# Kernel tuning notes

Measured on AMD Instinct MI355X. Metric: run time of the kernel, lower is better.

The kernel has to match this reference:

```python
import jax, jax.numpy as jnp
import numpy as np

B, Hs, Ws, ENC = 128, 14, 14, 2048
ATT, EMB, DEC, V, L = 512, 512, 512, 30000, 22


def setup_inputs() -> dict:
    key = jax.random.key(0)
    ks = jax.random.split(key, 16)
    u = lambda k, shape, a: jax.random.uniform(k, shape, jnp.float32, -a, a)
    cap_len_rest = jax.random.randint(ks[2], (B - 1, 1), 2, L + 1)
    caption_lengths = jnp.concatenate([jnp.array([[L]], dtype=cap_len_rest.dtype), cap_len_rest], axis=0)
    return {
        "encoder_out": jax.random.normal(ks[0], (B, Hs, Ws, ENC), jnp.float32),
        "encoded_captions": jax.random.randint(ks[1], (B, L), 0, V),
        "caption_lengths": caption_lengths,
        # learned parameters
        "emb_table": u(ks[3], (V, EMB), 0.1),
        "We": u(ks[4], (ENC, ATT), 0.02), "be": jnp.zeros((ATT,), jnp.float32),
        "Wd": u(ks[5], (DEC, ATT), 0.02), "bd": jnp.zeros((ATT,), jnp.float32),
        "wf": u(ks[6], (ATT,), 0.02), "bf": jnp.zeros((), jnp.float32),
        "W_ih": u(ks[7], (4 * DEC, EMB + ENC), 0.02), "b_ih": jnp.zeros((4 * DEC,), jnp.float32),
        "W_hh": u(ks[8], (4 * DEC, DEC), 0.02), "b_hh": jnp.zeros((4 * DEC,), jnp.float32),
        "W_fc": u(ks[9], (DEC, V), 0.1), "b_fc": jnp.zeros((V,), jnp.float32),
    }


def reference(encoder_out, encoded_captions, caption_lengths,
              emb_table, We, be, Wd, bd, wf, bf,
              W_ih, b_ih, W_hh, b_hh, W_fc, b_fc):
    Bsz = encoder_out.shape[0]
    enc = encoder_out.reshape(Bsz, -1, encoder_out.shape[-1])  # [B, P, ENC]
    lens = caption_lengths[:, 0]
    sort_ind = jnp.argsort(-lens)  # descending, stable
    lens = lens[sort_ind]
    enc = enc[sort_ind]
    caps = encoded_captions[sort_ind]
    emb = emb_table[caps]  # [B, L, EMB]
    dec_lens = lens - 1
    T = caps.shape[1] - 1  # static max(decode_lengths) (max length present in batch)
    D = W_hh.shape[1]

    attn1 = enc @ We + be  # [B, P, ATT], loop-invariant
    h0 = jnp.zeros((Bsz, D), enc.dtype)
    c0 = jnp.zeros((Bsz, D), enc.dtype)

    def step(carry, xs):
        h, c = carry
        emb_t, active = xs  # [B, EMB], [B] bool
        attn2 = h @ Wd + bd  # [B, ATT]
        e = jnp.einsum('bpa,a->bp', jax.nn.relu(attn1 + attn2[:, None, :]), wf) + bf
        alpha = jax.nn.softmax(e, axis=1)  # [B, P]
        ctx = jnp.einsum('bp,bpe->be', alpha, enc)  # [B, ENC]
        x = jnp.concatenate([emb_t, ctx], axis=1)
        gates = x @ W_ih.T + b_ih + h @ W_hh.T + b_hh
        i, f, g, o = jnp.split(gates, 4, axis=1)  # PyTorch LSTM gate order
        c_new = jax.nn.sigmoid(f) * c + jax.nn.sigmoid(i) * jnp.tanh(g)
        h_new = jax.nn.sigmoid(o) * jnp.tanh(c_new)
        m = active[:, None]
        h = jnp.where(m, h_new, h)
        c = jnp.where(m, c_new, c)
        out_t = jnp.where(m, h_new @ W_fc + b_fc, 0.0)  # [B, V]
        alpha_t = jnp.where(m, alpha, 0.0)
        return (h, c), (out_t, alpha_t)

    ts = jnp.arange(T)
    active = ts[:, None] < dec_lens[None, :]  # [T, B]
    emb_steps = jnp.transpose(emb[:, :T], (1, 0, 2))  # [T, B, EMB]
    (_, _), (outs, alphas) = jax.lax.scan(step, (h0, c0), (emb_steps, active))
    outputs = jnp.transpose(outs, (1, 0, 2))  # [B, T, V]
    alphas = jnp.transpose(alphas, (1, 0, 2))  # [B, T, P]
    return outputs, caps, dec_lens, alphas, sort_ind
```

## Files before the change

### kernel.cpp

```cpp
#include <hip/hip_runtime.h>
#include <cstdint>
#include <cstddef>

#define B_    128
#define P_    196
#define ENC_  2048
#define ATT_  512
#define DEC_  512
#define EMB_  512
#define V_    30000
#define L_    22
#define T_    21
#define KGATE (EMB_ + ENC_ + DEC_)
#define NGATE (4*DEC_)
#define KS    8
#define LDSK  40

typedef unsigned short u16;
typedef unsigned int   u32;
typedef float f32x4 __attribute__((ext_vector_type(4)));
typedef short s16x8 __attribute__((ext_vector_type(8)));

__device__ __forceinline__ u16 f2bf(float f){
  u32 u = __float_as_uint(f);
  u = (u + 0x7fffu + ((u >> 16) & 1u)) >> 16;
  return (u16)u;
}
__device__ __forceinline__ float bf2f(u16 h){
  return __uint_as_float(((u32)h) << 16);
}

template<int MODE>
__global__ __launch_bounds__(256)
void gemm_bf16(const u16* __restrict__ A, int lda,
               const u16* __restrict__ Bm, int N, int K, int M,
               const float* __restrict__ bias,
               u16* __restrict__ outb,
               float* __restrict__ outp,
               const int* __restrict__ declens)
{
  __shared__ __align__(16) u16 As[64*LDSK];
  __shared__ __align__(16) u16 Bs[64*LDSK];
  __shared__ __align__(16) float Cs[64*68];

  const int tid = threadIdx.x;
  const int nt = blockIdx.x * 64;
  const int mt = blockIdx.y * 64;
  int k0 = 0, k1 = K;
  if (MODE == 1){ int kl = K / KS; k0 = blockIdx.z * kl; k1 = k0 + kl; }

  f32x4 acc[4];
  #pragma unroll
  for (int s = 0; s < 4; s++) acc[s] = f32x4{0.f,0.f,0.f,0.f};

  const int am = tid >> 2;
  const int ak = (tid & 3) * 8;
  const int bk = tid >> 3;
  const int bn = (tid & 7) * 8;
  const int wv = tid >> 6;
  const int ln = tid & 63;
  const int qd = ln >> 4;
  const int lm = ln & 15;

  for (int kc = k0; kc < k1; kc += 32){
    uint4 av = *reinterpret_cast<const uint4*>(A + (size_t)(mt + am) * lda + kc + ak);
    *reinterpret_cast<uint4*>(&As[am * LDSK + ak]) = av;
    u16 bv[8];
    bool inb = true;
    if (MODE == 2) inb = (nt + bn + 8 <= N);
    if (inb){
      uint4 bq = *reinterpret_cast<const uint4*>(Bm + (size_t)(kc + bk) * N + nt + bn);
      bv[0]=(u16)(bq.x&0xffff); bv[1]=(u16)(bq.x>>16);
      bv[2]=(u16)(bq.y&0xffff); bv[3]=(u16)(bq.y>>16);
      bv[4]=(u16)(bq.z&0xffff); bv[5]=(u16)(bq.z>>16);
      bv[6]=(u16)(bq.w&0xffff); bv[7]=(u16)(bq.w>>16);
    } else {
      #pragma unroll
      for (int j=0;j<8;j++) bv[j]=0;
    }
    #pragma unroll
    for (int j=0;j<8;j++) Bs[(bn + j) * LDSK + bk] = bv[j];
    __syncthreads();

    s16x8 af = *reinterpret_cast<const s16x8*>(&As[(wv*16 + lm) * LDSK + qd*8]);
    #pragma unroll
    for (int s=0;s<4;s++){
      s16x8 bfr = *reinterpret_cast<const s16x8*>(&Bs[(s*16 + lm) * LDSK + qd*8]);
      acc[s] = __builtin_amdgcn_mfma_f32_16x16x32_bf16(af, bfr, acc[s], 0, 0, 0);
    }
    __syncthreads();
  }

  #pragma unroll
  for (int s=0;s<4;s++)
    #pragma unroll
    for (int r=0;r<4;r++)
      Cs[(wv*16 + qd*4 + r)*68 + s*16 + lm] = acc[s][r];
  __syncthreads();

  const int row = tid >> 2;
  const int cs0 = (tid & 3) * 16;
  if (MODE == 0){
    __align__(16) u16 pack[16];
    #pragma unroll
    for (int j=0;j<16;j++)
      pack[j] = f2bf(Cs[row*68 + cs0 + j] + bias[nt + cs0 + j]);
    uint4* dst = reinterpret_cast<uint4*>(outb + (size_t)(mt+row)*N + nt + cs0);
    dst[0] = *reinterpret_cast<uint4*>(pack);
    dst[1] = *reinterpret_cast<uint4*>(pack + 8);
  } else if (MODE == 1){
    float* dst = outp + (size_t)blockIdx.z * M * N + (size_t)(mt+row)*N + nt + cs0;
    #pragma unroll
    for (int j=0;j<4;j++){
      float4 v = { Cs[row*68+cs0+4*j], Cs[row*68+cs0+4*j+1],
                   Cs[row*68+cs0+4*j+2], Cs[row*68+cs0+4*j+3] };
      reinterpret_cast<float4*>(dst)[j] = v;
    }
  } else {
    int r = mt + row;
    int ti = r >> 7;
    int bb = r & 127;
    bool act = ti < declens[bb];
    float* dst = outp + ((size_t)bb * T_ + ti) * (size_t)V_ + nt + cs0;
    #pragma unroll
    for (int j=0;j<16;j++){
      int col = nt + cs0 + j;
      if (col < N) dst[j] = act ? (Cs[row*68 + cs0 + j] + bias[col]) : 0.f;
    }
  }
}

__global__ void cvt_bf16(const float* __restrict__ in, u16* __restrict__ out, int n4){
  int i = blockIdx.x * blockDim.x + threadIdx.x;
  int stride = gridDim.x * blockDim.x;
  for (; i < n4; i += stride){
    float4 v = reinterpret_cast<const float4*>(in)[i];
    __align__(8) u16 p[4] = {f2bf(v.x), f2bf(v.y), f2bf(v.z), f2bf(v.w)};
    reinterpret_cast<uint2*>(out)[i] = *reinterpret_cast<uint2*>(p);
  }
}

__global__ void build_bigb(const float* __restrict__ Wih, const float* __restrict__ Whh,
                           u16* __restrict__ out)
{
  __shared__ float tile[32][33];
  int k0 = blockIdx.x * 32, n0 = blockIdx.y * 32;
  int tx = threadIdx.x, ty = threadIdx.y;
  #pragma unroll
  for (int j=0;j<4;j++){
    int nl = ty + j*8;
    int n = n0 + nl, k = k0 + tx;
    float v = (k0 < 2560) ? Wih[(size_t)n*2560 + k] : Whh[(size_t)n*512 + (k - 2560)];
    tile[nl][tx] = v;
  }
  __syncthreads();
  #pragma unroll
  for (int j=0;j<4;j++){
    int kl = ty + j*8;
    out[(size_t)(k0 + kl)*NGATE + n0 + tx] = f2bf(tile[tx][kl]);
  }
}

__global__ void sort_kernel(const int* __restrict__ cap_len, const int* __restrict__ caps,
                            int* __restrict__ sortind, int* __restrict__ declens,
                            int* __restrict__ caps_s,
                            float* __restrict__ out_caps, float* __restrict__ out_declens,
                            float* __restrict__ out_sortind)
{
  __shared__ int si[B_];
  if (threadIdx.x == 0){
    int cnt = 0;
    for (int v = L_; v >= 0 && cnt < B_; v--)
      for (int b = 0; b < B_; b++)
        if (cap_len[b] == v) si[cnt++] = b;
  }
  __syncthreads();
  for (int i = threadIdx.x; i < B_; i += 256){
    int sb = si[i];
    sortind[i] = sb; out_sortind[i] = (float)sb;
    int dl = cap_len[sb] - 1;
    declens[i] = dl; out_declens[i] = (float)dl;
  }
  for (int i = threadIdx.x; i < B_*L_; i += 256){
    int bb = i / L_;
    int c = caps[si[bb]*L_ + (i % L_)];
    caps_s[i] = c; out_caps[i] = (float)c;
  }
}

__global__ void emb_fill(const float* __restrict__ emb_table, const int* __restrict__ caps_i,
                         u16* __restrict__ xa, int t)
{
  int b = blockIdx.x;
  int cap = caps_i[b*L_ + t];
  for (int k = threadIdx.x; k < EMB_; k += 256)
    xa[(size_t)b*KGATE + k] = f2bf(emb_table[(size_t)cap*EMB_ + k]);
}

__global__ __launch_bounds__(256)
void attn_esm(const u16* __restrict__ attn1, const float* __restrict__ a2part,
              const float* __restrict__ bd, const float* __restrict__ wf,
              const float* __restrict__ bfp,
              const int* __restrict__ sortind, const int* __restrict__ declens,
              float* __restrict__ alpha_buf, float* __restrict__ out_alphas, int t)
{
  __shared__ float a2[ATT_];
  __shared__ float wfs[ATT_];
  __shared__ float es[P_];
  __shared__ float red[8];
  int b = blockIdx.x, tid = threadIdx.x;
  for (int i = tid; i < ATT_; i += 256){
    float v = bd[i];
    #pragma unroll
    for (int s=0;s<KS;s++) v += a2part[((size_t)s*B_ + b)*ATT_ + i];
    a2[i] = v;
    wfs[i] = wf[i];
  }
  __syncthreads();
  int sb = sortind[b];
  const u16* arow = attn1 + (size_t)sb * P_ * ATT_;
  int wv = tid >> 6, ln = tid & 63;
  float bfv = bfp[0];
  for (int i = 0; i < P_/4; i++){
    int p = i*4 + wv;
    uint4 q = *reinterpret_cast<const uint4*>(arow + (size_t)p*ATT_ + ln*8);
    u32 wd_[4] = {q.x, q.y, q.z, q.w};
    float sum = 0.f;
    #pragma unroll
    for (int j=0;j<4;j++){
      int a0 = ln*8 + 2*j;
      float v0 = bf2f((u16)(wd_[j] & 0xffff)) + a2[a0];
      float v1 = bf2f((u16)(wd_[j] >> 16))    + a2[a0+1];
      sum += fmaxf(v0, 0.f) * wfs[a0];
      sum += fmaxf(v1, 0.f) * wfs[a0+1];
    }
    #pragma unroll
    for (int off=32; off; off>>=1) sum += __shfl_xor(sum, off);
    if (ln == 0) es[p] = sum + bfv;
  }
  __syncthreads();
  float m = (tid < P_) ? es[tid] : -1e30f;
  #pragma unroll
  for (int off=32; off; off>>=1) m = fmaxf(m, __shfl_xor(m, off));
  if (ln == 0) red[wv] = m;
  __syncthreads();
  m = fmaxf(fmaxf(red[0],red[1]), fmaxf(red[2],red[3]));
  float ev = (tid < P_) ? expf(es[tid] - m) : 0.f;
  float sm = ev;
  #pragma unroll
  for (int off=32; off; off>>=1) sm += __shfl_xor(sm, off);
  if (ln == 0) red[4+wv] = sm;
  __syncthreads();
  float tot = red[4]+red[5]+red[6]+red[7];
  if (tid < P_){
    float al = ev / tot;
    alpha_buf[b*P_ + tid] = al;
    out_alphas[((size_t)b*T_ + t)*P_ + tid] = (t < declens[b]) ? al : 0.f;
  }
}

__global__ __launch_bounds__(256)
void ctx_kernel(const u16* __restrict__ enc_bf, const float* __restrict__ alpha_buf,
                const int* __restrict__ sortind, u16* __restrict__ xa)
{
  __shared__ float al[P_];
  int b = blockIdx.x, ch = blockIdx.y, tid = threadIdx.x;
  for (int i = tid; i < P_; i += 256) al[i] = alpha_buf[b*P_ + i];
  __syncthreads();
  int sb = sortind[b];
  const u16* eb = enc_bf + (size_t)sb * P_ * ENC_ + ch * 1024 + tid * 4;
  float a0=0.f, a1=0.f, a2v=0.f, a3=0.f;
  #pragma unroll 4
  for (int p=0;p<P_;p++){
    uint2 q = *reinterpret_cast<const uint2*>(eb + (size_t)p * ENC_);
    float w = al[p];
    a0  += w * bf2f((u16)(q.x & 0xffff));
    a1  += w * bf2f((u16)(q.x >> 16));
    a2v += w * bf2f((u16)(q.y & 0xffff));
    a3  += w * bf2f((u16)(q.y >> 16));
  }
  __align__(8) u16 pk[4] = {f2bf(a0), f2bf(a1), f2bf(a2v), f2bf(a3)};
  *reinterpret_cast<uint2*>(xa + (size_t)b*KGATE + EMB_ + ch*1024 + tid*4) =
      *reinterpret_cast<uint2*>(pk);
}

__global__ __launch_bounds__(256)
void lstm_kernel(const float* __restrict__ gpart, const float* __restrict__ bih,
                 const float* __restrict__ bhh,
                 float* __restrict__ hf, float* __restrict__ cfb,
                 u16* __restrict__ xa, u16* __restrict__ Hh,
                 const int* __restrict__ declens, const int* __restrict__ caps_i,
                 const float* __restrict__ emb_table, int t)
{
  int b = blockIdx.x, tid = threadIdx.x;
  bool act = t < declens[b];
  #pragma unroll
  for (int j=0;j<2;j++){
    int n = j*256 + tid;
    float gi = bih[n]      + bhh[n];
    float gf = bih[n+512]  + bhh[n+512];
    float gg = bih[n+1024] + bhh[n+1024];
    float go = bih[n+1536] + bhh[n+1536];
    #pragma unroll
    for (int s=0;s<KS;s++){
      const float* gp = gpart + ((size_t)s*B_ + b)*NGATE;
      gi += gp[n]; gf += gp[n+512]; gg += gp[n+1024]; go += gp[n+1536];
    }
    float co = cfb[b*DEC_ + n];
    float iv = 1.f/(1.f + expf(-gi));
    float fv = 1.f/(1.f + expf(-gf));
    float gv = tanhf(gg);
    float ov = 1.f/(1.f + expf(-go));
    float cn = fv*co + iv*gv;
    float hn = ov * tanhf(cn);
    float ho = act ? hn : hf[b*DEC_ + n];
    float c2 = act ? cn : co;
    hf[b*DEC_ + n] = ho;
    cfb[b*DEC_ + n] = c2;
    u16 hb = f2bf(ho);
    xa[(size_t)b*KGATE + EMB_ + ENC_ + n] = hb;
    Hh[((size_t)t*B_ + b)*DEC_ + n] = hb;
  }
  if (t + 1 < T_){
    int cap = caps_i[b*L_ + t + 1];
    for (int k = tid; k < EMB_; k += 256)
      xa[(size_t)b*KGATE + k] = f2bf(emb_table[(size_t)cap*EMB_ + k]);
  }
}

extern "C" void kernel_launch(void* const* d_in, const int* in_sizes, int n_in,
                              void* d_out, int out_size, void* d_ws, size_t ws_size,
                              hipStream_t stream)
{
  (void)in_sizes; (void)n_in; (void)out_size; (void)ws_size;
  const float* enc  = (const float*)d_in[0];
  const int*   caps = (const int*)d_in[1];
  const int*   clen = (const int*)d_in[2];
  const float* embt = (const float*)d_in[3];
  const float* We   = (const float*)d_in[4];
  const float* be   = (const float*)d_in[5];
  const float* Wd   = (const float*)d_in[6];
  const float* bd   = (const float*)d_in[7];
  const float* wf   = (const float*)d_in[8];
  const float* bfp  = (const float*)d_in[9];
  const float* Wih  = (const float*)d_in[10];
  const float* bih  = (const float*)d_in[11];
  const float* Whh  = (const float*)d_in[12];
  const float* bhh  = (const float*)d_in[13];
  const float* Wfc  = (const float*)d_in[14];
  const float* bfc  = (const float*)d_in[15];

  float* out = (float*)d_out;
  float* out_outputs = out;
  float* out_caps    = out + (size_t)80640000;
  float* out_declens = out + (size_t)80640000 + 2816;
  float* out_alphas  = out + (size_t)80640000 + 2816 + 128;
  float* out_sortind = out + (size_t)80640000 + 2816 + 128 + 526848;

  char* w = (char*)d_ws;
  size_t off = 0;
  auto alloc = [&](size_t bytes)->char*{
    char* p = w + off; off += (bytes + 255) & ~(size_t)255; return p;
  };
  u16*  enc_bf = (u16*)alloc((size_t)B_*P_*ENC_*2);
  u16*  attn1  = (u16*)alloc((size_t)B_*P_*ATT_*2);
  u16*  We_bf  = (u16*)alloc((size_t)ENC_*ATT_*2);
  u16*  Wd_bf  = (u16*)alloc((size_t)DEC_*ATT_*2);
  u16*  BigB   = (u16*)alloc((size_t)KGATE*NGATE*2);
  u16*  Wfc_bf = (u16*)alloc((size_t)DEC_*V_*2);
  u16*  Hh     = (u16*)alloc((size_t)T_*B_*DEC_*2);
  float* hf    = (float*)alloc((size_t)B_*DEC_*4);
  float* cf    = (float*)alloc((size_t)B_*DEC_*4);
  u16*  xa     = (u16*)alloc((size_t)B_*KGATE*2);
  float* a2p   = (float*)alloc((size_t)KS*B_*ATT_*4);
  float* gp    = (float*)alloc((size_t)KS*B_*NGATE*4);
  float* albuf = (float*)alloc((size_t)B_*P_*4);
  int*  caps_i = (int*)alloc((size_t)B_*L_*4);
  int*  decl_i = (int*)alloc(512);
  int*  sort_i = (int*)alloc(512);

  hipMemsetAsync(hf, 0, (size_t)B_*DEC_*4*2 + (size_t)B_*KGATE*2, stream);

  sort_kernel<<<1, 256, 0, stream>>>(clen, caps, sort_i, decl_i, caps_i,
                                     out_caps, out_declens, out_sortind);
  emb_fill<<<B_, 256, 0, stream>>>(embt, caps_i, xa, 0);

  cvt_bf16<<<4096, 256, 0, stream>>>(enc, enc_bf, (int)((size_t)B_*P_*ENC_/4));
  cvt_bf16<<<512, 256, 0, stream>>>(We, We_bf, ENC_*ATT_/4);
  cvt_bf16<<<128, 256, 0, stream>>>(Wd, Wd_bf, DEC_*ATT_/4);
  cvt_bf16<<<2048, 256, 0, stream>>>(Wfc, Wfc_bf, DEC_*V_/4);
  build_bigb<<<dim3(KGATE/32, NGATE/32), dim3(32, 8), 0, stream>>>(Wih, Whh, BigB);

  gemm_bf16<0><<<dim3(ATT_/64, (B_*P_)/64), 256, 0, stream>>>(
      enc_bf, ENC_, We_bf, ATT_, ENC_, B_*P_, be, attn1, nullptr, nullptr);

  for (int t = 0; t < T_; t++){
    gemm_bf16<1><<<dim3(ATT_/64, B_/64, KS), 256, 0, stream>>>(
        xa + EMB_ + ENC_, KGATE, Wd_bf, ATT_, DEC_, B_, nullptr, nullptr, a2p, nullptr);
    attn_esm<<<B_, 256, 0, stream>>>(attn1, a2p, bd, wf, bfp, sort_i, decl_i,
                                     albuf, out_alphas, t);
    ctx_kernel<<<dim3(B_, 2), 256, 0, stream>>>(enc_bf, albuf, sort_i, xa);
    gemm_bf16<1><<<dim3(NGATE/64, B_/64, KS), 256, 0, stream>>>(
        xa, KGATE, BigB, NGATE, KGATE, B_, nullptr, nullptr, gp, nullptr);
    lstm_kernel<<<B_, 256, 0, stream>>>(gp, bih, bhh, hf, cf, xa, Hh,
                                        decl_i, caps_i, embt, t);
  }

  gemm_bf16<2><<<dim3((V_ + 63)/64, (T_*B_)/64), 256, 0, stream>>>(
      Hh, DEC_, Wfc_bf, V_, DEC_, T_*B_, bfc, nullptr, out_outputs, decl_i);
}
```

Baseline: 3.112 ms.

## Add 128x128 transposed-B GEMM with direct LDS loads for attn1 and FC

Adds a new bf16 MFMA GEMM that uses 128x128 block tiles, a 4x4 accumulator grid per wave, and a swizzled LDS layout filled by global_load_lds. It takes B pre-transposed to K-major. We and W_fc are now transposed and converted once, with W_fc padded to 30080 columns, and both the attention projection GEMM and the final vocabulary projection GEMM use the new kernel. The MODE 2 grid is ordered so that adjacent blocks share the same weight columns. The goal is more reuse per loaded tile and fewer LDS transposes on the two large GEMMs. The cost is larger register and LDS use and an extra transpose pass.

```diff
diff --git a/kernel.cpp b/kernel.cpp
--- a/kernel.cpp
+++ b/kernel.cpp
@@ -9,6 +9,7 @@
 #define DEC_  512
 #define EMB_  512
 #define V_    30000
+#define VPAD_ 30080
 #define L_    22
 #define T_    21
 #define KGATE (EMB_ + ENC_ + DEC_)
@@ -28,6 +29,132 @@
 }
 __device__ __forceinline__ float bf2f(u16 h){
   return __uint_as_float(((u32)h) << 16);
+}
+
+__device__ __forceinline__ void gload_lds16(const u16* g, u16* l){
+  __builtin_amdgcn_global_load_lds(
+      (const __attribute__((address_space(1))) void*)g,
+      (__attribute__((address_space(3))) void*)l, 16, 0, 0);
+}
+
+template<int MODE>
+__global__ __launch_bounds__(256)
+void gemm_bt(const u16* __restrict__ A,
+             const u16* __restrict__ Bt,
+             int N, int K,
+             const float* __restrict__ bias,
+             u16* __restrict__ outb,
+             float* __restrict__ outp,
+             const int* __restrict__ declens)
+{
+  __shared__ __align__(16) u16 As[128*32];
+  __shared__ __align__(16) u16 Bs[128*32];
+  __shared__ __align__(16) float Cs[32*132];
+
+  const int tid = threadIdx.x;
+  const int bxn = (MODE == 2) ? blockIdx.y : blockIdx.x;
+  const int bym = (MODE == 2) ? blockIdx.x : blockIdx.y;
+  const int nt = bxn * 128;
+  const size_t mt = (size_t)bym * 128;
+
+  const int wv = tid >> 6;
+  const int ln = tid & 63;
+  const int lm = ln & 15;
+  const int qd = ln >> 4;
+  const int wr = wv >> 1;
+  const int wc = wv & 1;
+
+  f32x4 acc[4][4];
+  #pragma unroll
+  for (int i=0;i<4;i++)
+    #pragma unroll
+    for (int j=0;j<4;j++) acc[i][j] = f32x4{0.f,0.f,0.f,0.f};
+
+  const int c0 = tid, c1 = 256 + tid;
+  const int ar0 = c0 >> 2, ac0 = (((c0 & 3) ^ ((ar0 >> 1) & 3)) * 8);
+  const int ar1 = c1 >> 2, ac1 = (((c1 & 3) ^ ((ar1 >> 1) & 3)) * 8);
+  const u16* Ab0 = A  + (mt + ar0) * (size_t)K + ac0;
+  const u16* Ab1 = A  + (mt + ar1) * (size_t)K + ac1;
+  const u16* Bb0 = Bt + ((size_t)nt + ar0) * (size_t)K + ac0;
+  const u16* Bb1 = Bt + ((size_t)nt + ar1) * (size_t)K + ac1;
+  u16* lA0 = As + (size_t)c0 * 8;
+  u16* lA1 = As + (size_t)c1 * 8;
+  u16* lB0 = Bs + (size_t)c0 * 8;
+  u16* lB1 = Bs + (size_t)c1 * 8;
+
+  int aoff[4], boff[4];
+  #pragma unroll
+  for (int i=0;i<4;i++){
+    int ra = wr*64 + i*16 + lm;
+    aoff[i] = ra*32 + ((qd ^ ((ra >> 1) & 3)) * 8);
+    int rb = wc*64 + i*16 + lm;
+    boff[i] = rb*32 + ((qd ^ ((rb >> 1) & 3)) * 8);
+  }
+
+  for (int kc = 0; kc < K; kc += 32){
+    gload_lds16(Ab0 + kc, lA0);
+    gload_lds16(Ab1 + kc, lA1);
+    gload_lds16(Bb0 + kc, lB0);
+    gload_lds16(Bb1 + kc, lB1);
+    __syncthreads();
+    s16x8 af[4], bfr[4];
+    #pragma unroll
+    for (int i=0;i<4;i++) af[i]  = *reinterpret_cast<const s16x8*>(As + aoff[i]);
+    #pragma unroll
+    for (int i=0;i<4;i++) bfr[i] = *reinterpret_cast<const s16x8*>(Bs + boff[i]);
+    #pragma unroll
+    for (int i=0;i<4;i++)
+      #pragma unroll
+      for (int j=0;j<4;j++)
+        acc[i][j] = __builtin_amdgcn_mfma_f32_16x16x32_bf16(af[i], bfr[j], acc[i][j], 0, 0, 0);
+    __syncthreads();
+  }
+
+  #pragma unroll
+  for (int mi=0; mi<4; mi++){
+    const int lrb = wr*16 + qd*4;
+    #pragma unroll
+    for (int ni=0; ni<4; ni++)
+      #pragma unroll
+      for (int rr=0; rr<4; rr++)
+        Cs[(lrb+rr)*132 + wc*64 + ni*16 + lm] = acc[mi][ni][rr];
+    __syncthreads();
+    const int er = tid >> 3;
+    const int ec = (tid & 7) * 16;
+    const size_t grow = mt + (size_t)(er >> 4)*64 + mi*16 + (er & 15);
+    const float* cr = Cs + er*132 + ec;
+    if (MODE == 0){
+      __align__(16) u16 pk[16];
+      #pragma unroll
+      for (int j=0;j<16;j++) pk[j] = f2bf(cr[j] + bias[nt + ec + j]);
+      uint4* dst = reinterpret_cast<uint4*>(outb + grow*(size_t)N + nt + ec);
+      dst[0] = *reinterpret_cast<uint4*>(pk);
+      dst[1] = *reinterpret_cast<uint4*>(pk + 8);
+    } else {
+      const int ti = (int)(grow >> 7);
+      const int bb = (int)(grow & 127);
+      const bool act = ti < declens[bb];
+      float* dst = outp + ((size_t)bb*T_ + ti)*(size_t)V_ + nt + ec;
+      if (nt + 128 <= N){
+        #pragma unroll
+        for (int j=0;j<4;j++){
+          float4 v;
+          v.x = act ? cr[4*j+0] + bias[nt+ec+4*j+0] : 0.f;
+          v.y = act ? cr[4*j+1] + bias[nt+ec+4*j+1] : 0.f;
+          v.z = act ? cr[4*j+2] + bias[nt+ec+4*j+2] : 0.f;
+          v.w = act ? cr[4*j+3] + bias[nt+ec+4*j+3] : 0.f;
+          reinterpret_cast<float4*>(dst)[j] = v;
+        }
+      } else {
+        #pragma unroll
+        for (int j=0;j<16;j++){
+          int col = nt + ec + j;
+          if (col < N) dst[j] = act ? cr[j] + bias[col] : 0.f;
+        }
+      }
+    }
+    __syncthreads();
+  }
 }
 
 template<int MODE>
@@ -66,18 +193,11 @@
     uint4 av = *reinterpret_cast<const uint4*>(A + (size_t)(mt + am) * lda + kc + ak);
     *reinterpret_cast<uint4*>(&As[am * LDSK + ak]) = av;
     u16 bv[8];
-    bool inb = true;
-    if (MODE == 2) inb = (nt + bn + 8 <= N);
-    if (inb){
-      uint4 bq = *reinterpret_cast<const uint4*>(Bm + (size_t)(kc + bk) * N + nt + bn);
-      bv[0]=(u16)(bq.x&0xffff); bv[1]=(u16)(bq.x>>16);
-      bv[2]=(u16)(bq.y&0xffff); bv[3]=(u16)(bq.y>>16);
-      bv[4]=(u16)(bq.z&0xffff); bv[5]=(u16)(bq.z>>16);
-      bv[6]=(u16)(bq.w&0xffff); bv[7]=(u16)(bq.w>>16);
-    } else {
-      #pragma unroll
-      for (int j=0;j<8;j++) bv[j]=0;
-    }
+    uint4 bq = *reinterpret_cast<const uint4*>(Bm + (size_t)(kc + bk) * N + nt + bn);
+    bv[0]=(u16)(bq.x&0xffff); bv[1]=(u16)(bq.x>>16);
+    bv[2]=(u16)(bq.y&0xffff); bv[3]=(u16)(bq.y>>16);
+    bv[4]=(u16)(bq.z&0xffff); bv[5]=(u16)(bq.z>>16);
+    bv[6]=(u16)(bq.w&0xffff); bv[7]=(u16)(bq.w>>16);
     #pragma unroll
     for (int j=0;j<8;j++) Bs[(bn + j) * LDSK + bk] = bv[j];
     __syncthreads();
@@ -100,32 +220,13 @@
 
   const int row = tid >> 2;
   const int cs0 = (tid & 3) * 16;
-  if (MODE == 0){
-    __align__(16) u16 pack[16];
-    #pragma unroll
-    for (int j=0;j<16;j++)
-      pack[j] = f2bf(Cs[row*68 + cs0 + j] + bias[nt + cs0 + j]);
-    uint4* dst = reinterpret_cast<uint4*>(outb + (size_t)(mt+row)*N + nt + cs0);
-    dst[0] = *reinterpret_cast<uint4*>(pack);
-    dst[1] = *reinterpret_cast<uint4*>(pack + 8);
-  } else if (MODE == 1){
+  if (MODE == 1){
     float* dst = outp + (size_t)blockIdx.z * M * N + (size_t)(mt+row)*N + nt + cs0;
     #pragma unroll
     for (int j=0;j<4;j++){
       float4 v = { Cs[row*68+cs0+4*j], Cs[row*68+cs0+4*j+1],
                    Cs[row*68+cs0+4*j+2], Cs[row*68+cs0+4*j+3] };
       reinterpret_cast<float4*>(dst)[j] = v;
-    }
-  } else {
-    int r = mt + row;
-    int ti = r >> 7;
-    int bb = r & 127;
-    bool act = ti < declens[bb];
-    float* dst = outp + ((size_t)bb * T_ + ti) * (size_t)V_ + nt + cs0;
-    #pragma unroll
-    for (int j=0;j<16;j++){
-      int col = nt + cs0 + j;
-      if (col < N) dst[j] = act ? (Cs[row*68 + cs0 + j] + bias[col]) : 0.f;
     }
   }
 }
@@ -137,6 +238,25 @@
     float4 v = reinterpret_cast<const float4*>(in)[i];
     __align__(8) u16 p[4] = {f2bf(v.x), f2bf(v.y), f2bf(v.z), f2bf(v.w)};
     reinterpret_cast<uint2*>(out)[i] = *reinterpret_cast<uint2*>(p);
+  }
+}
+
+__global__ void transpose_cvt(const float* __restrict__ in, u16* __restrict__ out,
+                              int K, int N)
+{
+  __shared__ float tile[32][33];
+  int n0 = blockIdx.x * 32, k0 = blockIdx.y * 32;
+  int tx = threadIdx.x, ty = threadIdx.y;
+  #pragma unroll
+  for (int j=0;j<4;j++){
+    int k = k0 + ty + j*8, n = n0 + tx;
+    tile[ty + j*8][tx] = (n < N) ? in[(size_t)k*N + n] : 0.f;
+  }
+  __syncthreads();
+  #pragma unroll
+  for (int j=0;j<4;j++){
+    int nl = ty + j*8;
+    out[(size_t)(n0 + nl)*K + k0 + tx] = f2bf(tile[tx][nl]);
   }
 }
 
@@ -364,10 +484,10 @@
   };
   u16*  enc_bf = (u16*)alloc((size_t)B_*P_*ENC_*2);
   u16*  attn1  = (u16*)alloc((size_t)B_*P_*ATT_*2);
-  u16*  We_bf  = (u16*)alloc((size_t)ENC_*ATT_*2);
+  u16*  WeT    = (u16*)alloc((size_t)ATT_*ENC_*2);
   u16*  Wd_bf  = (u16*)alloc((size_t)DEC_*ATT_*2);
   u16*  BigB   = (u16*)alloc((size_t)KGATE*NGATE*2);
-  u16*  Wfc_bf = (u16*)alloc((size_t)DEC_*V_*2);
+  u16*  WfcT   = (u16*)alloc((size_t)VPAD_*DEC_*2);
   u16*  Hh     = (u16*)alloc((size_t)T_*B_*DEC_*2);
   float* hf    = (float*)alloc((size_t)B_*DEC_*4);
   float* cf    = (float*)alloc((size_t)B_*DEC_*4);
@@ -386,13 +506,13 @@
   emb_fill<<<B_, 256, 0, stream>>>(embt, caps_i, xa, 0);
 
   cvt_bf16<<<4096, 256, 0, stream>>>(enc, enc_bf, (int)((size_t)B_*P_*ENC_/4));
-  cvt_bf16<<<512, 256, 0, stream>>>(We, We_bf, ENC_*ATT_/4);
   cvt_bf16<<<128, 256, 0, stream>>>(Wd, Wd_bf, DEC_*ATT_/4);
-  cvt_bf16<<<2048, 256, 0, stream>>>(Wfc, Wfc_bf, DEC_*V_/4);
+  transpose_cvt<<<dim3(ATT_/32, ENC_/32), dim3(32, 8), 0, stream>>>(We, WeT, ENC_, ATT_);
+  transpose_cvt<<<dim3(VPAD_/32, DEC_/32), dim3(32, 8), 0, stream>>>(Wfc, WfcT, DEC_, V_);
   build_bigb<<<dim3(KGATE/32, NGATE/32), dim3(32, 8), 0, stream>>>(Wih, Whh, BigB);
 
-  gemm_bf16<0><<<dim3(ATT_/64, (B_*P_)/64), 256, 0, stream>>>(
-      enc_bf, ENC_, We_bf, ATT_, ENC_, B_*P_, be, attn1, nullptr, nullptr);
+  gemm_bt<0><<<dim3(ATT_/128, (B_*P_)/128), 256, 0, stream>>>(
+      enc_bf, WeT, ATT_, ENC_, be, attn1, nullptr, nullptr);
 
   for (int t = 0; t < T_; t++){
     gemm_bf16<1><<<dim3(ATT_/64, B_/64, KS), 256, 0, stream>>>(
@@ -406,6 +526,6 @@
                                         decl_i, caps_i, embt, t);
   }
 
-  gemm_bf16<2><<<dim3((V_ + 63)/64, (T_*B_)/64), 256, 0, stream>>>(
-      Hh, DEC_, Wfc_bf, V_, DEC_, T_*B_, bfc, nullptr, out_outputs, decl_i);
-}
+  gemm_bt<2><<<dim3((T_*B_)/128, VPAD_/128), 256, 0, stream>>>(
+      Hh, WfcT, V_, DEC_, bfc, nullptr, out_outputs, decl_i);
+}
```

New measurement: 2.643 ms. 15.1% less time.
